# Optimization experiments

Measured on AMD Instinct MI355X. Metric: run time of the kernel, lower is better.

The kernel has to match this reference:

```python
import jax, jax.numpy as jnp
import numpy as np

WIN = 7            # skimage default win_size
NP_ = WIN * WIN    # pixels per 2D window (per channel)
COV_NORM = NP_ / (NP_ - 1.0)  # use_sample_covariance=True
K1, K2 = 0.01, 0.03


def setup_inputs() -> dict:
    key = jax.random.key(0)
    k1, k2 = jax.random.split(key)
    img1 = jax.random.uniform(k1, (32, 3, 512, 512), dtype=jnp.float32)
    img2 = jax.random.uniform(k2, (32, 3, 512, 512), dtype=jnp.float32)
    return {"img1": img1, "img2": img2}


def _uf(x):
    # valid 7x7 uniform (mean) filter; x: [N, 1, H, W] -> [N, 1, H-6, W-6]
    # independent of boundary mode.
    k = jnp.ones((1, 1, WIN, WIN), x.dtype) / NP_
    return jax.lax.conv_general_dilated(
        x, k, window_strides=(1, 1), padding='VALID',
        dimension_numbers=('NCHW', 'OIHW', 'NCHW'))


def reference(img1, img2):
    B, C, H, W = img1.shape
    x = img1.reshape(B * C, 1, H, W)
    y = img2.reshape(B * C, 1, H, W)

    ux, uy = _uf(x), _uf(y)
    uxx, uyy, uxy = _uf(x * x), _uf(y * y), _uf(x * y)
    vx = COV_NORM * (uxx - ux * ux)
    vy = COV_NORM * (uyy - uy * uy)
    vxy = COV_NORM * (uxy - ux * uy)

    # per-image data_range = img2[i].max() - img2[i].min() (over C,H,W)
    dr = jnp.max(img2, axis=(1, 2, 3)) - jnp.min(img2, axis=(1, 2, 3))  # [B]
    dr = jnp.repeat(dr, C).reshape(B * C, 1, 1, 1)
    C1 = (K1 * dr) ** 2
    C2 = (K2 * dr) ** 2

    S = ((2.0 * ux * uy + C1) * (2.0 * vxy + C2)) / \
        ((ux * ux + uy * uy + C1) * (vx + vy + C2))

    # skimage: mean over cropped map per channel, mean over channels, then batch mean
    ssim_per_img = S.reshape(B, C, H - WIN + 1, W - WIN + 1).mean(axis=(1, 2, 3))
    return 1.0 - ssim_per_img.mean()
```

## Files before the change

kernel.cpp:

```cpp
#include <hip/hip_runtime.h>

#define IMG_H 512
#define IMG_W 512
#define NIMG 96
#define WOUT 506
#define STRIP 23
#define NSTRIPS 22
#define TOTAL_VALS 24579456.0f

__device__ __forceinline__ unsigned fkey(float f){
    unsigned b = __float_as_uint(f);
    return (b & 0x80000000u) ? ~b : (b | 0x80000000u);
}
__device__ __forceinline__ float fdec(unsigned k){
    unsigned b = (k & 0x80000000u) ? (k ^ 0x80000000u) : ~k;
    return __uint_as_float(b);
}

__global__ __launch_bounds__(256) void minmax_kernel(const float4* __restrict__ y4,
                                                     unsigned* __restrict__ maxk,
                                                     unsigned* __restrict__ mink){
    int blk  = blockIdx.x;
    int img  = blk >> 3;
    int chnk = blk & 7;
    const float4* base = y4 + (size_t)img * (786432/4) + (size_t)chnk * 24576;
    float mn = 3.4e38f, mx = -3.4e38f;
    for (int i = threadIdx.x; i < 24576; i += 256){
        float4 v = base[i];
        mn = fminf(mn, fminf(fminf(v.x, v.y), fminf(v.z, v.w)));
        mx = fmaxf(mx, fmaxf(fmaxf(v.x, v.y), fmaxf(v.z, v.w)));
    }
    #pragma unroll
    for (int off = 32; off; off >>= 1){
        mn = fminf(mn, __shfl_down(mn, off));
        mx = fmaxf(mx, __shfl_down(mx, off));
    }
    if ((threadIdx.x & 63) == 0){
        atomicMax(&maxk[img], fkey(mx));
        atomicMin(&mink[img], fkey(mn));
    }
}


#define ROWOP(row, OPA) { \
    const float* xr = x + (size_t)(row)*IMG_W + c0; \
    const float* yr = y + (size_t)(row)*IMG_W + c0; \
    float4 xa = *(const float4*)xr;     float4 xb = *(const float4*)(xr+4); \
    float4 ya = *(const float4*)yr;     float4 yb = *(const float4*)(yr+4); \
    float xv[8] = {xa.x,xa.y,xa.z,xa.w,xb.x,xb.y,xb.z,xb.w}; \
    float yv[8] = {ya.x,ya.y,ya.z,ya.w,yb.x,yb.y,yb.z,yb.w}; \
    _Pragma("unroll") \
    for (int k = 0; k < 8; k++){ \
        sx[k]  OPA xv[k]; \
        sy[k]  OPA yv[k]; \
        sxx[k] OPA xv[k]*xv[k]; \
        syy[k] OPA yv[k]*yv[k]; \
        sxy[k] OPA xv[k]*yv[k]; \
    } }

#define HWIN(q, outw) { \
    float4 ha = *(float4*)&cs[q][c0];    float4 hb = *(float4*)&cs[q][c0+4]; \
    float4 hc = *(float4*)&cs[q][c0+8];  float4 hd = *(float4*)&cs[q][c0+12]; \
    float h[16] = {ha.x,ha.y,ha.z,ha.w, hb.x,hb.y,hb.z,hb.w, \
                   hc.x,hc.y,hc.z,hc.w, hd.x,hd.y,hd.z,hd.w}; \
    float w = h[0]+h[1]+h[2]+h[3]+h[4]+h[5]+h[6]; \
    outw[0] = w; \
    _Pragma("unroll") \
    for (int j = 1; j < 8; j++){ w += h[j+6] - h[j-1]; outw[j] = w; } }

__global__ __launch_bounds__(64) void ssim_kernel(const float* __restrict__ img1,
                                                  const float* __restrict__ img2,
                                                  const unsigned* __restrict__ maxk,
                                                  const unsigned* __restrict__ mink,
                                                  float* __restrict__ acc){
    __shared__ float cs[5][520];

    int img   = blockIdx.x % NIMG;
    int strip = blockIdx.x / NIMG;
    int b     = img / 3;

    float dr = fdec(maxk[b]) - fdec(mink[b]);
    float c1 = 0.01f * dr;  c1 *= c1;
    float c2 = 0.03f * dr;  c2 *= c2;

    const float* x = img1 + (size_t)img * (IMG_H*IMG_W);
    const float* y = img2 + (size_t)img * (IMG_H*IMG_W);

    int t  = threadIdx.x;
    int c0 = t * 8;

    float sx[8]={0,0,0,0,0,0,0,0}, sy[8]={0,0,0,0,0,0,0,0};
    float sxx[8]={0,0,0,0,0,0,0,0}, syy[8]={0,0,0,0,0,0,0,0}, sxy[8]={0,0,0,0,0,0,0,0};

    int r0 = strip * STRIP;

    for (int rr = 0; rr < 7; rr++){ ROWOP(r0+rr, +=) }

    float accS = 0.0f;

    for (int r = r0; r < r0 + STRIP; r++){
        *(float4*)&cs[0][c0]   = make_float4(sx[0],sx[1],sx[2],sx[3]);
        *(float4*)&cs[0][c0+4] = make_float4(sx[4],sx[5],sx[6],sx[7]);
        *(float4*)&cs[1][c0]   = make_float4(sy[0],sy[1],sy[2],sy[3]);
        *(float4*)&cs[1][c0+4] = make_float4(sy[4],sy[5],sy[6],sy[7]);
        *(float4*)&cs[2][c0]   = make_float4(sxx[0],sxx[1],sxx[2],sxx[3]);
        *(float4*)&cs[2][c0+4] = make_float4(sxx[4],sxx[5],sxx[6],sxx[7]);
        *(float4*)&cs[3][c0]   = make_float4(syy[0],syy[1],syy[2],syy[3]);
        *(float4*)&cs[3][c0+4] = make_float4(syy[4],syy[5],syy[6],syy[7]);
        *(float4*)&cs[4][c0]   = make_float4(sxy[0],sxy[1],sxy[2],sxy[3]);
        *(float4*)&cs[4][c0+4] = make_float4(sxy[4],sxy[5],sxy[6],sxy[7]);
        __syncthreads();

        float wsx[8], wsy[8], wsxx[8], wsyy[8], wsxy[8];
        HWIN(0, wsx)  HWIN(1, wsy)  HWIN(2, wsxx)  HWIN(3, wsyy)  HWIN(4, wsxy)
        __syncthreads();

        const float inv  = 1.0f/49.0f;
        const float covn = 49.0f/48.0f;
        #pragma unroll
        for (int j = 0; j < 8; j++){
            if (c0 + j < WOUT){
                float ux  = wsx[j]*inv,  uy  = wsy[j]*inv;
                float exx = wsxx[j]*inv, eyy = wsyy[j]*inv, exy = wsxy[j]*inv;
                float vx  = covn*(exx - ux*ux);
                float vy  = covn*(eyy - uy*uy);
                float vxy = covn*(exy - ux*uy);
                float a1 = 2.0f*ux*uy + c1,        a2 = 2.0f*vxy + c2;
                float b1 = ux*ux + uy*uy + c1,     b2 = vx + vy + c2;
                accS += (a1*a2) / (b1*b2);
            }
        }

        if (r < r0 + STRIP - 1){
            ROWOP(r+7, +=)
            ROWOP(r,   -=)
        }
    }

    #pragma unroll
    for (int off = 32; off; off >>= 1)
        accS += __shfl_down(accS, off);
    if (t == 0)
        atomicAdd(acc, accS);
}

__global__ void finalize_kernel(const float* __restrict__ acc, float* __restrict__ out){
    out[0] = 1.0f - acc[0] * (1.0f / TOTAL_VALS);
}

extern "C" void kernel_launch(void* const* d_in, const int* in_sizes, int n_in,
                              void* d_out, int out_size, void* d_ws, size_t ws_size,
                              hipStream_t stream) {
    const float* img1 = (const float*)d_in[0];
    const float* img2 = (const float*)d_in[1];
    float* out = (float*)d_out;

    char* ws = (char*)d_ws;
    float*    acc  = (float*)ws;
    unsigned* maxk = (unsigned*)(ws + 128);
    unsigned* mink = (unsigned*)(ws + 256);

    hipMemsetAsync(ws, 0, 256, stream);
    hipMemsetAsync(ws + 256, 0xFF, 128, stream);

    minmax_kernel<<<256, 256, 0, stream>>>((const float4*)img2, maxk, mink);
    ssim_kernel<<<NSTRIPS*NIMG, 64, 0, stream>>>(img1, img2, maxk, mink, acc);
    finalize_kernel<<<1, 1, 0, stream>>>(acc, out);
}
```

Before: 316.2 us.

## Replace LDS horizontal window with shuffles, shrink strips, simplify SSIM algebra

The horizontal 7-wide window sum now reads its neighbouring columns from the adjacent lane with wave shuffles instead of staging column sums through shared memory, which removes the two barriers per row. Strip height is halved to produce more blocks, and block indices are remapped across images. The SSIM formula is rewritten on unscaled sums with folded constants and uses a hardware reciprocal instead of a divide. The minmax kernel gets 8x more blocks. In exchange, the shorter strips add more vertical warm-up rows, and the reciprocal is approximate.

New measurement: 356.5 us. +12.8%, slower.

```diff
diff --git a/kernel.cpp b/kernel.cpp
--- a/kernel.cpp
+++ b/kernel.cpp
@@ -4,8 +4,9 @@
 #define IMG_W 512
 #define NIMG 96
 #define WOUT 506
-#define STRIP 23
-#define NSTRIPS 22
+#define STRIP 11
+#define NSTRIPS 46
+#define NBLK (NSTRIPS*NIMG)
 #define TOTAL_VALS 24579456.0f
 
 __device__ __forceinline__ unsigned fkey(float f){
@@ -21,11 +22,11 @@
                                                      unsigned* __restrict__ maxk,
                                                      unsigned* __restrict__ mink){
     int blk  = blockIdx.x;
-    int img  = blk >> 3;
-    int chnk = blk & 7;
-    const float4* base = y4 + (size_t)img * (786432/4) + (size_t)chnk * 24576;
+    int img  = blk >> 6;
+    int chnk = blk & 63;
+    const float4* base = y4 + (size_t)img * 196608 + (size_t)chnk * 3072;
     float mn = 3.4e38f, mx = -3.4e38f;
-    for (int i = threadIdx.x; i < 24576; i += 256){
+    for (int i = threadIdx.x; i < 3072; i += 256){
         float4 v = base[i];
         mn = fminf(mn, fminf(fminf(v.x, v.y), fminf(v.z, v.w)));
         mx = fmaxf(mx, fmaxf(fmaxf(v.x, v.y), fmaxf(v.z, v.w)));
@@ -58,30 +59,37 @@
         sxy[k] OPA xv[k]*yv[k]; \
     } }
 
-#define HWIN(q, outw) { \
-    float4 ha = *(float4*)&cs[q][c0];    float4 hb = *(float4*)&cs[q][c0+4]; \
-    float4 hc = *(float4*)&cs[q][c0+8];  float4 hd = *(float4*)&cs[q][c0+12]; \
-    float h[16] = {ha.x,ha.y,ha.z,ha.w, hb.x,hb.y,hb.z,hb.w, \
-                   hc.x,hc.y,hc.z,hc.w, hd.x,hd.y,hd.z,hd.w}; \
-    float w = h[0]+h[1]+h[2]+h[3]+h[4]+h[5]+h[6]; \
-    outw[0] = w; \
-    _Pragma("unroll") \
-    for (int j = 1; j < 8; j++){ w += h[j+6] - h[j-1]; outw[j] = w; } }
+#define HSHUF(s, outw) { \
+    float n0=__shfl_down(s[0],1), n1=__shfl_down(s[1],1), n2=__shfl_down(s[2],1); \
+    float n3=__shfl_down(s[3],1), n4=__shfl_down(s[4],1), n5=__shfl_down(s[5],1); \
+    float w = s[0]+s[1]+s[2]+s[3]+s[4]+s[5]+s[6]; \
+    outw[0]=w; \
+    w += s[7]-s[0]; outw[1]=w; \
+    w += n0-s[1];   outw[2]=w; \
+    w += n1-s[2];   outw[3]=w; \
+    w += n2-s[3];   outw[4]=w; \
+    w += n3-s[4];   outw[5]=w; \
+    w += n4-s[5];   outw[6]=w; \
+    w += n5-s[6];   outw[7]=w; }
 
 __global__ __launch_bounds__(64) void ssim_kernel(const float* __restrict__ img1,
                                                   const float* __restrict__ img2,
                                                   const unsigned* __restrict__ maxk,
                                                   const unsigned* __restrict__ mink,
                                                   float* __restrict__ acc){
-    __shared__ float cs[5][520];
-
-    int img   = blockIdx.x % NIMG;
-    int strip = blockIdx.x / NIMG;
+    int bid = blockIdx.x;
+    int L   = (bid & 7) * (NBLK/8) + (bid >> 3);
+    int img   = L / NSTRIPS;
+    int strip = L - img * NSTRIPS;
     int b     = img / 3;
 
     float dr = fdec(maxk[b]) - fdec(mink[b]);
     float c1 = 0.01f * dr;  c1 *= c1;
     float c2 = 0.03f * dr;  c2 *= c2;
+    const float c1s = 2401.0f * c1;
+    const float c2s = 2401.0f * c2;
+    const float CO2 = 2.0f * 49.0f / 48.0f;
+    const float COV = 49.0f / 48.0f;
 
     const float* x = img1 + (size_t)img * (IMG_H*IMG_W);
     const float* y = img2 + (size_t)img * (IMG_H*IMG_W);
@@ -99,35 +107,23 @@
     float accS = 0.0f;
 
     for (int r = r0; r < r0 + STRIP; r++){
-        *(float4*)&cs[0][c0]   = make_float4(sx[0],sx[1],sx[2],sx[3]);
-        *(float4*)&cs[0][c0+4] = make_float4(sx[4],sx[5],sx[6],sx[7]);
-        *(float4*)&cs[1][c0]   = make_float4(sy[0],sy[1],sy[2],sy[3]);
-        *(float4*)&cs[1][c0+4] = make_float4(sy[4],sy[5],sy[6],sy[7]);
-        *(float4*)&cs[2][c0]   = make_float4(sxx[0],sxx[1],sxx[2],sxx[3]);
-        *(float4*)&cs[2][c0+4] = make_float4(sxx[4],sxx[5],sxx[6],sxx[7]);
-        *(float4*)&cs[3][c0]   = make_float4(syy[0],syy[1],syy[2],syy[3]);
-        *(float4*)&cs[3][c0+4] = make_float4(syy[4],syy[5],syy[6],syy[7]);
-        *(float4*)&cs[4][c0]   = make_float4(sxy[0],sxy[1],sxy[2],sxy[3]);
-        *(float4*)&cs[4][c0+4] = make_float4(sxy[4],sxy[5],sxy[6],sxy[7]);
-        __syncthreads();
+        float wsx[8], wsy[8], wsxx[8], wsyy[8], wsxy[8];
+        HSHUF(sx, wsx)  HSHUF(sy, wsy)  HSHUF(sxx, wsxx)
+        HSHUF(syy, wsyy)  HSHUF(sxy, wsxy)
 
-        float wsx[8], wsy[8], wsxx[8], wsyy[8], wsxy[8];
-        HWIN(0, wsx)  HWIN(1, wsy)  HWIN(2, wsxx)  HWIN(3, wsyy)  HWIN(4, wsxy)
-        __syncthreads();
-
-        const float inv  = 1.0f/49.0f;
-        const float covn = 49.0f/48.0f;
         #pragma unroll
         for (int j = 0; j < 8; j++){
             if (c0 + j < WOUT){
-                float ux  = wsx[j]*inv,  uy  = wsy[j]*inv;
-                float exx = wsxx[j]*inv, eyy = wsyy[j]*inv, exy = wsxy[j]*inv;
-                float vx  = covn*(exx - ux*ux);
-                float vy  = covn*(eyy - uy*uy);
-                float vxy = covn*(exy - ux*uy);
-                float a1 = 2.0f*ux*uy + c1,        a2 = 2.0f*vxy + c2;
-                float b1 = ux*ux + uy*uy + c1,     b2 = vx + vy + c2;
-                accS += (a1*a2) / (b1*b2);
+                float P = wsx[j], Q = wsy[j];
+                float t1 = P*Q;
+                float t2 = fmaf(P, P, Q*Q);
+                float a1 = fmaf(2.0f, t1, c1s);
+                float b1 = t2 + c1s;
+                float u  = fmaf(49.0f, wsxy[j], -t1);
+                float a2 = fmaf(CO2, u, c2s);
+                float v  = fmaf(49.0f, wsxx[j]+wsyy[j], -t2);
+                float b2 = fmaf(COV, v, c2s);
+                accS += (a1*a2) * __builtin_amdgcn_rcpf(b1*b2);
             }
         }
 
@@ -163,7 +159,7 @@
     hipMemsetAsync(ws, 0, 256, stream);
     hipMemsetAsync(ws + 256, 0xFF, 128, stream);
 
-    minmax_kernel<<<256, 256, 0, stream>>>((const float4*)img2, maxk, mink);
-    ssim_kernel<<<NSTRIPS*NIMG, 64, 0, stream>>>(img1, img2, maxk, mink, acc);
+    minmax_kernel<<<2048, 256, 0, stream>>>((const float4*)img2, maxk, mink);
+    ssim_kernel<<<NBLK, 64, 0, stream>>>(img1, img2, maxk, mink, acc);
     finalize_kernel<<<1, 1, 0, stream>>>(acc, out);
 }
```
